# Kernel optimization log

Hardware: AMD Instinct MI355X
Metric: run time of the kernel (lower is better)

## Reference

```python
import jax, jax.numpy as jnp
import numpy as np

ITERATIONS = 20


def _affine_sample(canvas, theta):
    """PyTorch-equivalent F.affine_grid + F.grid_sample (bilinear,
    align_corners=False, padding_mode='zeros') for all T transforms at once.
    canvas: [H, W], theta: [T, 2, 3] -> returns [T, H, W].
    """
    H, W = canvas.shape
    dt = canvas.dtype
    # Normalized base grid coords, align_corners=False: centers of pixels.
    xs = (jnp.arange(W, dtype=dt) * 2 + 1) / W - 1  # [W]
    ys = (jnp.arange(H, dtype=dt) * 2 + 1) / H - 1  # [H]
    # Sampled normalized coords: [x', y'] = theta @ [x, y, 1]
    gx = (theta[:, 0, 0, None, None] * xs[None, None, :]
          + theta[:, 0, 1, None, None] * ys[None, :, None]
          + theta[:, 0, 2, None, None])  # [T, H, W]
    gy = (theta[:, 1, 0, None, None] * xs[None, None, :]
          + theta[:, 1, 1, None, None] * ys[None, :, None]
          + theta[:, 1, 2, None, None])  # [T, H, W]
    # Unnormalize to pixel coords (align_corners=False).
    ix = (gx + 1) * (W * 0.5) - 0.5
    iy = (gy + 1) * (H * 0.5) - 0.5
    x0f = jnp.floor(ix)
    y0f = jnp.floor(iy)
    wx1 = ix - x0f
    wy1 = iy - y0f
    wx0 = 1 - wx1
    wy0 = 1 - wy1
    x0 = x0f.astype(jnp.int32)
    y0 = y0f.astype(jnp.int32)

    def corner(xi, yi):
        valid = (xi >= 0) & (xi < W) & (yi >= 0) & (yi < H)
        v = canvas[jnp.clip(yi, 0, H - 1), jnp.clip(xi, 0, W - 1)]
        return jnp.where(valid, v, jnp.zeros((), dt))  # zeros padding

    return (wx0 * wy0 * corner(x0, y0)
            + wx1 * wy0 * corner(x0 + 1, y0)
            + wx0 * wy1 * corner(x0, y0 + 1)
            + wx1 * wy1 * corner(x0 + 1, y0 + 1))


def setup_inputs() -> dict:
    key = jax.random.key(0)
    k1, k2, k3 = jax.random.split(key, 3)
    H, W, T = 1024, 1024, 16
    canvas0 = jax.random.uniform(k1, (H, W), dtype=jnp.float32)
    theta = jax.random.normal(k2, (T, 2, 3), dtype=jnp.float32)
    probs = jax.random.uniform(k3, (T,), dtype=jnp.float32)
    base_value = jnp.zeros((1,), dtype=jnp.float32)
    return {"canvas0": canvas0, "theta": theta, "probs": probs,
            "base_value": base_value}


def reference(canvas0, theta, probs, base_value):
    p = probs / jnp.sum(probs)

    def step(canvas, _):
        sampled = _affine_sample(canvas, theta)          # [T, H, W]
        new_canvas = jnp.einsum('t,thw->hw', p, sampled)  # weighted IFS sum
        return new_canvas, None

    canvas, _ = jax.lax.scan(step, canvas0, None, length=ITERATIONS)
    return canvas + base_value[0]
```

## Files before the change

kernel.cpp:

```cpp
#include <hip/hip_runtime.h>

constexpr int W = 1024;
constexpr int H = 1024;
constexpr int T = 16;
constexpr int ITERS = 20;
constexpr int P2 = 1040;
constexpr int ROWS2 = 1027;
constexpr int ALLOC2F = ROWS2 * P2 * 2;
constexpr int TILES_X = W / 16;
constexpr int TILES_Y = H / 16;
constexpr int NTILES = TILES_X * TILES_Y;

typedef float f2 __attribute__((ext_vector_type(2), aligned(8)));
typedef float f4 __attribute__((ext_vector_type(4), aligned(8)));

__global__ void setup_coef(const float* __restrict__ theta,
                           const float* __restrict__ probs,
                           float* __restrict__ coef) {
    int t = threadIdx.x;
    if (t >= T) return;
    float sum = 0.f;
    for (int i = 0; i < T; ++i) sum += probs[i];
    float p = probs[t] / sum;
    const float* th = theta + 6 * t;
    float a = th[0], b = th[1], c = th[2];
    float d = th[3], e = th[4], f = th[5];
    float Cx = a * ((1.0f - (float)W) * 0.5f)
             + b * ((1.0f - (float)H) * 0.5f)
             + (c + 1.0f) * ((float)W * 0.5f) - 0.5f;
    float Cy = d * ((1.0f - (float)W) * 0.5f)
             + e * ((1.0f - (float)H) * 0.5f)
             + (f + 1.0f) * ((float)H * 0.5f) - 0.5f;
    float* o = coef + 8 * t;
    o[0] = p;  o[1] = a;  o[2] = b;  o[3] = Cx + 2.0f;
    o[4] = d;  o[5] = e;  o[6] = Cy + 2.0f; o[7] = 0.f;
}

__global__ __launch_bounds__(256) void setup_tiles(const float* __restrict__ coef,
                                                   float* __restrict__ tbl,
                                                   int* __restrict__ tcnt) {
    int tile = blockIdx.x * 256 + threadIdx.x;
    if (tile >= NTILES) return;
    int tx = tile & (TILES_X - 1), ty = tile >> 6;
    float w0 = (float)(tx * 16), w1 = w0 + 15.f;
    float h0 = (float)(ty * 16), h1 = h0 + 15.f;
    float* o = tbl + tile * 128;
    int n = 0;
    for (int t = 0; t < T; ++t) {
        const float* c = coef + t * 8;
        float Ax = c[1], Bx = c[2], Cx = c[3];
        float Ay = c[4], By = c[5], Cy = c[6];
        float xmin = Cx + (Ax >= 0.f ? Ax * w0 : Ax * w1) + (Bx >= 0.f ? Bx * h0 : Bx * h1);
        float xmax = Cx + (Ax >= 0.f ? Ax * w1 : Ax * w0) + (Bx >= 0.f ? Bx * h1 : Bx * h0);
        float ymin = Cy + (Ay >= 0.f ? Ay * w0 : Ay * w1) + (By >= 0.f ? By * h0 : By * h1);
        float ymax = Cy + (Ay >= 0.f ? Ay * w1 : Ay * w0) + (By >= 0.f ? By * h1 : By * h0);
        bool hit = !(xmax <= 1.f || xmin >= (float)(W + 2) ||
                     ymax <= 1.f || ymin >= (float)(H + 2));
        if (hit) {
            for (int j = 0; j < 8; ++j) o[n * 8 + j] = c[j];
            ++n;
        }
    }
    tcnt[tile] = n;
    int np = (n + 3) & ~3;
    for (int s = n; s < np; ++s)
        for (int j = 0; j < 8; ++j) o[s * 8 + j] = 0.f;
}

__global__ __launch_bounds__(256) void copy_in(const float* __restrict__ src,
                                               float* __restrict__ dstf) {
    int i = blockIdx.x * 256 + threadIdx.x;
    int h = i >> 10, w = i & 1023;
    float v = src[i];
    int c = w + 2;
    dstf[(((h + 2) * P2) + c) * 2 + 0] = v;
    dstf[(((h + 1) * P2) + c) * 2 + 1] = v;
}

template <int K>
__device__ __forceinline__ void ifs_body(const float* __restrict__ tc, int g,
                                         const f2* __restrict__ gb,
                                         float wf, float hf, float& acc) {
    float fx[K], fy[K], pp[K];
    int off[K];
    unsigned long long lv[K];
#pragma unroll
    for (int k = 0; k < K; ++k) {
        const float* c = tc + (g + k) * 8;
        float p = c[0], Ax = c[1], Bx = c[2], Cx = c[3];
        float Ay = c[4], By = c[5], Cy = c[6];
        float xb = fmaf(Ax, wf, fmaf(Bx, hf, Cx));
        float yb = fmaf(Ay, wf, fmaf(By, hf, Cy));
        bool live = (xb > 1.f) & (xb < 1026.f) & (yb > 1.f) & (yb < 1026.f);
        lv[k] = __ballot(live);
        float xc = fminf(fmaxf(xb, 0.f), 1037.f);
        float yc = fminf(fmaxf(yb, 0.f), 1026.f);
        float xi = floorf(xc), yi = floorf(yc);
        fx[k] = xc - xi;
        fy[k] = yc - yi;
        int o = (int)fmaf(yi, (float)P2, xi);
        off[k] = live ? o : 0;
        pp[k] = p;
    }
    f4 q[K];
#pragma unroll
    for (int k = 0; k < K; ++k) {
        if (lv[k]) q[k] = *(const f4*)(gb + off[k]);
        else       q[k] = f4{0.f, 0.f, 0.f, 0.f};
    }
#pragma unroll
    for (int k = 0; k < K; ++k) {
        float top = fmaf(fx[k], q[k].z - q[k].x, q[k].x);
        float bot = fmaf(fx[k], q[k].w - q[k].y, q[k].y);
        acc = fmaf(pp[k], fmaf(fy[k], bot - top, top), acc);
    }
}

__global__ __launch_bounds__(256) void ifs_iter(const float* __restrict__ inf,
                                                float* __restrict__ dstf,
                                                const float* __restrict__ tbl,
                                                const int* __restrict__ tcnt,
                                                const float* __restrict__ base,
                                                int last) {
    int tile = blockIdx.y * TILES_X + blockIdx.x;
    const float* tc = tbl + tile * 128;
    int np = (tcnt[tile] + 3) & ~3;

    int lid = threadIdx.x;
    int lane = lid & 63, wv = lid >> 6;
    int w = (blockIdx.x << 4) + ((wv & 1) << 3) + (lane & 7);
    int h = (blockIdx.y << 4) + ((wv >> 1) << 3) + (lane >> 3);
    float wf = (float)w, hf = (float)h;
    const f2* gb = (const f2*)inf;

    float acc = 0.f;
    int g = 0;
    for (; g + 8 <= np; g += 8) ifs_body<8>(tc, g, gb, wf, hf, acc);
    if (g < np)                 ifs_body<4>(tc, g, gb, wf, hf, acc);

    if (last) {
        dstf[(h << 10) + w] = acc + base[0];
    } else {
        int c = w + 2;
        dstf[(((h + 2) * P2) + c) * 2 + 0] = acc;
        dstf[(((h + 1) * P2) + c) * 2 + 1] = acc;
    }
}

extern "C" void kernel_launch(void* const* d_in, const int* in_sizes, int n_in,
                              void* d_out, int out_size, void* d_ws, size_t ws_size,
                              hipStream_t stream) {
    const float* canvas0 = (const float*)d_in[0];
    const float* theta   = (const float*)d_in[1];
    const float* probs   = (const float*)d_in[2];
    const float* base    = (const float*)d_in[3];

    float* raw   = (float*)d_ws;
    float* bufAf = raw;
    float* bufBf = raw + ALLOC2F;
    float* coef  = raw + 2 * ALLOC2F;
    float* tbl   = coef + T * 8;
    int*   tcnt  = (int*)(tbl + NTILES * 128);

    hipMemsetAsync(raw, 0, (size_t)2 * ALLOC2F * sizeof(float), stream);

    setup_coef<<<1, 64, 0, stream>>>(theta, probs, coef);
    setup_tiles<<<(NTILES + 255) / 256, 256, 0, stream>>>(coef, tbl, tcnt);
    copy_in<<<(H * W) / 256, 256, 0, stream>>>(canvas0, bufAf);

    dim3 block(256);
    dim3 grid(TILES_X, TILES_Y);

    const float* cur = bufAf;
    for (int i = 0; i < ITERS; ++i) {
        bool last = (i == ITERS - 1);
        float* dst = last ? (float*)d_out : ((i & 1) ? bufAf : bufBf);
        ifs_iter<<<grid, block, 0, stream>>>(cur, dst, tbl, tcnt, base,
                                             last ? 1 : 0);
        cur = dst;
    }
}
```

Baseline: 374.0 us.

## Pick per-transform wavefront footprint shape to minimize gather cache lines

For each transform, setup_coef picks one of three wavefront pixel-footprint shapes (4x16, 8x8, 16x4). It chooses the shape whose transformed footprint touches the fewest rows and cache lines of the source canvas. The tile table groups transforms by shape. The iteration kernel runs each group with a different thread-to-pixel mapping and gathers the partial sums through shared memory. This is meant to cut scattered gather traffic for strongly anisotropic transforms, at the cost of extra __syncthreads, LDS accumulation and less uniform loop trip counts.

```diff
diff --git a/kernel.cpp b/kernel.cpp
--- a/kernel.cpp
+++ b/kernel.cpp
@@ -10,6 +10,7 @@
 constexpr int TILES_X = W / 16;
 constexpr int TILES_Y = H / 16;
 constexpr int NTILES = TILES_X * TILES_Y;
+constexpr int TSTR = 256;
 
 typedef float f2 __attribute__((ext_vector_type(2), aligned(8)));
 typedef float f4 __attribute__((ext_vector_type(4), aligned(8)));
@@ -31,21 +32,29 @@
     float Cy = d * ((1.0f - (float)W) * 0.5f)
              + e * ((1.0f - (float)H) * 0.5f)
              + (f + 1.0f) * ((float)H * 0.5f) - 0.5f;
+    float ax = fabsf(a), bx = fabsf(b), ay = fabsf(d), by = fabsf(e);
+    int best_s = 3; float best = 3.4e38f;
+    for (int s = 2; s <= 4; ++s) {
+        float pw = (float)(1 << s), ph = (float)(64 >> s);
+        float rows = pw * ay + ph * by + 2.f;
+        float rowbytes = (pw * ax + ph * bx + 2.f) * 8.f + 8.f;
+        float score = rows * (1.f + rowbytes * (1.f / 64.f));
+        if (score < best) { best = score; best_s = s; }
+    }
     float* o = coef + 8 * t;
     o[0] = p;  o[1] = a;  o[2] = b;  o[3] = Cx + 2.0f;
-    o[4] = d;  o[5] = e;  o[6] = Cy + 2.0f; o[7] = 0.f;
+    o[4] = d;  o[5] = e;  o[6] = Cy + 2.0f;
+    o[7] = __int_as_float(best_s);
 }
 
 __global__ __launch_bounds__(256) void setup_tiles(const float* __restrict__ coef,
-                                                   float* __restrict__ tbl,
-                                                   int* __restrict__ tcnt) {
+                                                   float* __restrict__ tbl) {
     int tile = blockIdx.x * 256 + threadIdx.x;
     if (tile >= NTILES) return;
     int tx = tile & (TILES_X - 1), ty = tile >> 6;
     float w0 = (float)(tx * 16), w1 = w0 + 15.f;
     float h0 = (float)(ty * 16), h1 = h0 + 15.f;
-    float* o = tbl + tile * 128;
-    int n = 0;
+    int list[3][T]; int n[3] = {0, 0, 0};
     for (int t = 0; t < T; ++t) {
         const float* c = coef + t * 8;
         float Ax = c[1], Bx = c[2], Cx = c[3];
@@ -57,14 +66,31 @@
         bool hit = !(xmax <= 1.f || xmin >= (float)(W + 2) ||
                      ymax <= 1.f || ymin >= (float)(H + 2));
         if (hit) {
-            for (int j = 0; j < 8; ++j) o[n * 8 + j] = c[j];
-            ++n;
+            int s = __float_as_int(c[7]);
+            list[s - 2][n[s - 2]++] = t;
         }
     }
-    tcnt[tile] = n;
-    int np = (n + 3) & ~3;
-    for (int s = n; s < np; ++s)
-        for (int j = 0; j < 8; ++j) o[s * 8 + j] = 0.f;
+    float* o = tbl + tile * TSTR;
+    int pos = 8;
+    int np[3];
+    for (int b = 0; b < 3; ++b) {
+        int nb = n[b];
+        int nbp = (nb + 3) & ~3;
+        np[b] = nbp;
+        for (int i = 0; i < nb; ++i) {
+            const float* c = coef + list[b][i] * 8;
+            for (int j = 0; j < 8; ++j) o[pos + j] = c[j];
+            pos += 8;
+        }
+        for (int i = nb; i < nbp; ++i) {
+            for (int j = 0; j < 8; ++j) o[pos + j] = 0.f;
+            pos += 8;
+        }
+    }
+    o[0] = __int_as_float(np[0]);
+    o[1] = __int_as_float(np[1]);
+    o[2] = __int_as_float(np[2]);
+    for (int j = 3; j < 8; ++j) o[j] = 0.f;
 }
 
 __global__ __launch_bounds__(256) void copy_in(const float* __restrict__ src,
@@ -116,34 +142,61 @@
     }
 }
 
+template <int S>
+__device__ __forceinline__ void run_shape(const float* __restrict__ tc, int n,
+                                          const f2* __restrict__ gb,
+                                          int tbw, int tbh, int lane, int wv,
+                                          float* __restrict__ lacc) {
+    if (n == 0) return;
+    constexpr int pw = 1 << S;
+    int dw = lane & (pw - 1), dh = lane >> S;
+    int sw = wv << S;
+    int ow = sw & 15, oh = (sw >> 4) << (6 - S);
+    int px = ow + dw, py = oh + dh;
+    float wf = (float)(tbw + px), hf = (float)(tbh + py);
+
+    float accR = 0.f;
+    int g = 0;
+    for (; g + 8 <= n; g += 8) ifs_body<8>(tc, g, gb, wf, hf, accR);
+    if (g < n)                 ifs_body<4>(tc, g, gb, wf, hf, accR);
+
+    __syncthreads();
+    lacc[(py << 4) | px] += accR;
+}
+
 __global__ __launch_bounds__(256) void ifs_iter(const float* __restrict__ inf,
                                                 float* __restrict__ dstf,
                                                 const float* __restrict__ tbl,
-                                                const int* __restrict__ tcnt,
                                                 const float* __restrict__ base,
                                                 int last) {
+    __shared__ float lacc[256];
+
     int tile = blockIdx.y * TILES_X + blockIdx.x;
-    const float* tc = tbl + tile * 128;
-    int np = (tcnt[tile] + 3) & ~3;
+    const float* hdr = tbl + tile * TSTR;
+    int n2 = __float_as_int(hdr[0]);
+    int n3 = __float_as_int(hdr[1]);
+    int n4 = __float_as_int(hdr[2]);
+    const float* tc = hdr + 8;
 
     int lid = threadIdx.x;
     int lane = lid & 63, wv = lid >> 6;
-    int w = (blockIdx.x << 4) + ((wv & 1) << 3) + (lane & 7);
-    int h = (blockIdx.y << 4) + ((wv >> 1) << 3) + (lane >> 3);
-    float wf = (float)w, hf = (float)h;
+    int tbw = blockIdx.x << 4, tbh = blockIdx.y << 4;
     const f2* gb = (const f2*)inf;
 
-    float acc = 0.f;
-    int g = 0;
-    for (; g + 8 <= np; g += 8) ifs_body<8>(tc, g, gb, wf, hf, acc);
-    if (g < np)                 ifs_body<4>(tc, g, gb, wf, hf, acc);
-
+    lacc[lid] = 0.f;
+    run_shape<2>(tc, n2, gb, tbw, tbh, lane, wv, lacc);
+    run_shape<3>(tc + n2 * 8, n3, gb, tbw, tbh, lane, wv, lacc);
+    run_shape<4>(tc + (n2 + n3) * 8, n4, gb, tbw, tbh, lane, wv, lacc);
+    __syncthreads();
+
+    float v = lacc[lid];
+    int w = tbw + (lid & 15), h = tbh + (lid >> 4);
     if (last) {
-        dstf[(h << 10) + w] = acc + base[0];
+        dstf[(h << 10) + w] = v + base[0];
     } else {
         int c = w + 2;
-        dstf[(((h + 2) * P2) + c) * 2 + 0] = acc;
-        dstf[(((h + 1) * P2) + c) * 2 + 1] = acc;
+        dstf[(((h + 2) * P2) + c) * 2 + 0] = v;
+        dstf[(((h + 1) * P2) + c) * 2 + 1] = v;
     }
 }
 
@@ -160,12 +213,11 @@
     float* bufBf = raw + ALLOC2F;
     float* coef  = raw + 2 * ALLOC2F;
     float* tbl   = coef + T * 8;
-    int*   tcnt  = (int*)(tbl + NTILES * 128);
 
     hipMemsetAsync(raw, 0, (size_t)2 * ALLOC2F * sizeof(float), stream);
 
     setup_coef<<<1, 64, 0, stream>>>(theta, probs, coef);
-    setup_tiles<<<(NTILES + 255) / 256, 256, 0, stream>>>(coef, tbl, tcnt);
+    setup_tiles<<<(NTILES + 255) / 256, 256, 0, stream>>>(coef, tbl);
     copy_in<<<(H * W) / 256, 256, 0, stream>>>(canvas0, bufAf);
 
     dim3 block(256);
@@ -175,7 +227,7 @@
     for (int i = 0; i < ITERS; ++i) {
         bool last = (i == ITERS - 1);
         float* dst = last ? (float*)d_out : ((i & 1) ? bufAf : bufBf);
-        ifs_iter<<<grid, block, 0, stream>>>(cur, dst, tbl, tcnt, base,
+        ifs_iter<<<grid, block, 0, stream>>>(cur, dst, tbl, base,
                                              last ? 1 : 0);
         cur = dst;
     }
```

Measured after the change: 483.0 us. 29.2% more time.
